# Optimization experiments

Measured on AMD Instinct MI355X. Metric: run time of the kernel, lower is better.

The kernel has to match this reference:

```python
import jax, jax.numpy as jnp
import numpy as np

I = 128  # input_size
B, T = 64, 512
SIZES = [(I, 2*I), (2*I, 4*I), (4*I, 8*I), (8*I, 4*I), (4*I, 2*I), (2*I, I)]


def gru_layer(x, Wih, Whh):
    # x: [B,T,Din], Wih: [3H,Din], Whh: [3H,H]. PyTorch GRU, bias=False, h0=0.
    Bb, Tt, _ = x.shape
    H = Whh.shape[1]
    xg = jnp.einsum('bti,gi->btg', x, Wih)  # precompute input projections [B,T,3H]

    def step(h, xt):
        hg = h @ Whh.T                      # [B,3H]
        xr, xz, xn = jnp.split(xt, 3, axis=-1)
        hr, hz, hn = jnp.split(hg, 3, axis=-1)
        r = jax.nn.sigmoid(xr + hr)
        z = jax.nn.sigmoid(xz + hz)
        n = jnp.tanh(xn + r * hn)
        h_new = (1.0 - z) * n + z * h
        return h_new, h_new

    h0 = jnp.zeros((Bb, H), x.dtype)
    _, ys = jax.lax.scan(step, h0, jnp.swapaxes(xg, 0, 1))  # [T,B,H]
    return jnp.swapaxes(ys, 0, 1)


def layer_norm(x, g, b):
    # eps=0 as in the original module
    m = jnp.mean(x, axis=-1, keepdims=True)
    v = jnp.mean(jnp.square(x - m), axis=-1, keepdims=True)
    return (x - m) * jax.lax.rsqrt(v) * g + b


def setup_inputs() -> dict:
    key = jax.random.key(0)
    keys = jax.random.split(key, 1 + 2 * len(SIZES))
    inp = {'x': jax.random.normal(keys[0], (B, T, I), dtype=jnp.float32)}
    for l, (din, h) in enumerate(SIZES):
        s_ih = 1.0 / np.sqrt(h)
        inp[f'Wih{l}'] = jax.random.uniform(keys[1 + 2 * l], (3 * h, din), jnp.float32, -s_ih, s_ih)
        inp[f'Whh{l}'] = jax.random.uniform(keys[2 + 2 * l], (3 * h, h), jnp.float32, -s_ih, s_ih)
        inp[f'g{l}'] = jnp.ones((h,), jnp.float32)
        inp[f'b{l}'] = jnp.zeros((h,), jnp.float32)
    return inp


def reference(x,
              Wih0, Whh0, g0, b0,
              Wih1, Whh1, g1, b1,
              Wih2, Whh2, g2, b2,
              Wih3, Whh3, g3, b3,
              Wih4, Whh4, g4, b4,
              Wih5, Whh5, g5, b5):
    h = x
    params = [(Wih0, Whh0, g0, b0), (Wih1, Whh1, g1, b1), (Wih2, Whh2, g2, b2),
              (Wih3, Whh3, g3, b3), (Wih4, Whh4, g4, b4), (Wih5, Whh5, g5, b5)]
    for Wih, Whh, g, b in params:
        h = layer_norm(gru_layer(h, Wih, Whh), g, b)
    return h
```

## Files before the change

### kernel.cpp

```cpp
#include <hip/hip_runtime.h>
#include <stdint.h>

#define TT 512
#define BB 64
#define MM (BB * TT)

typedef short bf16x8 __attribute__((ext_vector_type(8)));
typedef float f32x4  __attribute__((ext_vector_type(4)));

#define LNP ((size_t)MM * 1024)

__device__ __align__(256) float g_xg[(size_t)MM * 3072];
__device__ __align__(256) unsigned short g_hex[176160768];
__device__ __align__(256) unsigned short g_ln[2 * LNP];
__device__ __align__(256) unsigned short g_w[18579456];
__device__ unsigned g_cnt[6 * TT * 8 * 16];

__device__ __forceinline__ float bf2f(unsigned short u) {
  union { unsigned int i; float f; } c; c.i = ((unsigned int)u) << 16; return c.f;
}
__device__ __forceinline__ unsigned short f2bf(float f) {
  union { float f; unsigned int i; } c; c.f = f;
  unsigned int u = c.i;
  return (unsigned short)((u + 0x7FFFu + ((u >> 16) & 1u)) >> 16);
}

__device__ __forceinline__ void gload16(const void* g, void* l) {
  __builtin_amdgcn_global_load_lds(
      (const __attribute__((address_space(1))) unsigned int*)g,
      (__attribute__((address_space(3))) unsigned int*)l, 16, 0, 0);
}

__global__ void __launch_bounds__(256) k_zero() {
  int i = blockIdx.x * 256 + threadIdx.x;
  int st = gridDim.x * 256;
  for (; i < 6 * TT * 8 * 16; i += st) g_cnt[i] = 0;
}

__global__ void __launch_bounds__(256) k_cvt_split(const float* __restrict__ s, int n,
                                                   int offh, int offl) {
  int i = blockIdx.x * 256 + threadIdx.x;
  int st = gridDim.x * 256;
  for (; i < n; i += st) {
    float v = s[i];
    unsigned short hi = f2bf(v);
    g_w[offh + i] = hi;
    g_w[offl + i] = f2bf(v - bf2f(hi));
  }
}
__global__ void __launch_bounds__(256) k_cvt_x(const float* __restrict__ s, int n) {
  int i = blockIdx.x * 256 + threadIdx.x;
  int st = gridDim.x * 256;
  for (; i < n; i += st) {
    float v = s[i];
    unsigned short hi = f2bf(v);
    g_ln[i] = hi;
    g_ln[LNP + i] = f2bf(v - bf2f(hi));
  }
}

__global__ void __launch_bounds__(256) k_gemm(int N, int K, int bhoff, int bloff) {
  __shared__ char sm[65536];
  char* Ah = sm;
  char* Al = sm + 16384;
  char* Bh = sm + 32768;
  char* Bl = sm + 49152;
  const unsigned short* A0 = g_ln;
  const unsigned short* A1 = g_ln + LNP;
  const unsigned short* B0 = g_w + bhoff;
  const unsigned short* B1 = g_w + bloff;
  const int tid = threadIdx.x;
  const int lane = tid & 63;
  const int w = tid >> 6;
  const int wm = w >> 1, wn = w & 1;
  const int m0 = blockIdx.x * 128, n0 = blockIdx.y * 128;
  const int c16 = lane & 15, r4 = lane >> 4;

  f32x4 acc[4][4];
#pragma unroll
  for (int i = 0; i < 4; ++i)
#pragma unroll
    for (int j = 0; j < 4; ++j) acc[i][j] = {0.f, 0.f, 0.f, 0.f};

  for (int k0 = 0; k0 < K; k0 += 64) {
    __syncthreads();
#pragma unroll
    for (int i = 0; i < 4; ++i) {
      int c = i * 256 + tid;
      int row = c >> 3, ch = c & 7;
      size_t ao = (size_t)(m0 + row) * K + k0 + ch * 8;
      size_t bo = (size_t)(n0 + row) * K + k0 + ch * 8;
      gload16(A0 + ao, Ah + c * 16);
      gload16(A1 + ao, Al + c * 16);
      gload16(B0 + bo, Bh + c * 16);
      gload16(B1 + bo, Bl + c * 16);
    }
    __syncthreads();
#pragma unroll
    for (int ks = 0; ks < 2; ++ks) {
      bf16x8 avh[4], avl[4], bvh[4], bvl[4];
#pragma unroll
      for (int mt = 0; mt < 4; ++mt) {
        int o = (wm * 64 + mt * 16 + c16) * 128 + ks * 64 + r4 * 16;
        avh[mt] = *(const bf16x8*)(Ah + o);
        avl[mt] = *(const bf16x8*)(Al + o);
      }
#pragma unroll
      for (int nt = 0; nt < 4; ++nt) {
        int o = (wn * 64 + nt * 16 + c16) * 128 + ks * 64 + r4 * 16;
        bvh[nt] = *(const bf16x8*)(Bh + o);
        bvl[nt] = *(const bf16x8*)(Bl + o);
      }
#pragma unroll
      for (int mt = 0; mt < 4; ++mt)
#pragma unroll
        for (int nt = 0; nt < 4; ++nt) {
          acc[mt][nt] = __builtin_amdgcn_mfma_f32_16x16x32_bf16(avh[mt], bvh[nt], acc[mt][nt], 0, 0, 0);
          acc[mt][nt] = __builtin_amdgcn_mfma_f32_16x16x32_bf16(avl[mt], bvh[nt], acc[mt][nt], 0, 0, 0);
          acc[mt][nt] = __builtin_amdgcn_mfma_f32_16x16x32_bf16(avh[mt], bvl[nt], acc[mt][nt], 0, 0, 0);
        }
    }
  }
#pragma unroll
  for (int mt = 0; mt < 4; ++mt)
#pragma unroll
    for (int nt = 0; nt < 4; ++nt) {
      int col = n0 + wn * 64 + nt * 16 + c16;
#pragma unroll
      for (int q = 0; q < 4; ++q) {
        int row = m0 + wm * 64 + mt * 16 + r4 * 4 + q;
        g_xg[(size_t)row * N + col] = acc[mt][nt][q];
      }
    }
}

template <int H, int NCOL, int NBLK, int NG>
__global__ void __launch_bounds__(256) k_scan(int whoff, int wloff,
                                              unsigned long long hoff, int coff) {
  constexpr int RB = 2 * H;
  constexpr int KI = H / 32;
  constexpr int ROWS = 3 * NCOL;
  constexpr int PL = ROWS * RB;
  constexpr unsigned TGT = NBLK / NG;
  __shared__ char lds[2 * PL];
  unsigned short* hexh = g_hex + hoff;
  unsigned short* hexl = hexh + (size_t)TT * BB * H;
  const int tid = threadIdx.x;
  const int lane = tid & 63;
  const int w = tid >> 6;
  const int bid = blockIdx.x;
  const int jb = bid * NCOL;
  const int c16 = lane & 15, r4 = lane >> 4;

  {
    constexpr int CPR = RB / 16;
    const unsigned short* wh = g_w + whoff;
    const unsigned short* wl = g_w + wloff;
    for (int c = tid; c < ROWS * CPR; c += 256) {
      int r = c / CPR, ch = c % CPR;
      int p = r / NCOL, j = r % NCOL;
      size_t so = (size_t)(p * H + jb + j) * H + ch * 8;
      int byte = (ch * 16) ^ ((r & 7) << 4);
      *(float4*)(lds + r * RB + byte) = *(const float4*)(wh + so);
      *(float4*)(lds + PL + r * RB + byte) = *(const float4*)(wl + so);
    }
  }
  __syncthreads();

  float hprev[4] = {0.f, 0.f, 0.f, 0.f};
  const int rA = c16 & (NCOL - 1);
  const int grp = bid & (NG - 1);

  for (int t = 0; t < TT; ++t) {
    float xr[4], xz[4], xn[4];
    if (NCOL == 16 || c16 < NCOL) {
#pragma unroll
      for (int q = 0; q < 4; ++q) {
        int b = w * 16 + r4 * 4 + q;
        size_t xo = ((size_t)b * TT + t) * (3 * H) + jb + c16;
        xr[q] = g_xg[xo];
        xz[q] = g_xg[xo + H];
        xn[q] = g_xg[xo + 2 * H];
      }
    } else {
#pragma unroll
      for (int q = 0; q < 4; ++q) { xr[q] = 0.f; xz[q] = 0.f; xn[q] = 0.f; }
    }

    f32x4 acc[3];
#pragma unroll
    for (int g = 0; g < 3; ++g) acc[g] = {0.f, 0.f, 0.f, 0.f};

    if (t > 0) {
      if (tid < 64) {
        const unsigned* cp = g_cnt + ((size_t)(coff + t - 1) * 8) * 16;
        for (;;) {
          unsigned v = (lane < NG)
              ? __hip_atomic_load(cp + lane * 16, __ATOMIC_RELAXED, __HIP_MEMORY_SCOPE_AGENT)
              : TGT;
          if (__all(v >= TGT)) break;
        }
      }
      __builtin_amdgcn_fence(__ATOMIC_ACQUIRE, "agent");
      __syncthreads();

      const unsigned short* hrh = hexh + ((size_t)(t - 1) * BB + (w * 16 + c16)) * H + r4 * 8;
      const unsigned short* hrl = hexl + ((size_t)(t - 1) * BB + (w * 16 + c16)) * H + r4 * 8;
#pragma unroll 4
      for (int ki = 0; ki < KI; ++ki) {
        bf16x8 ah = *(const bf16x8*)(hrh + ki * 32);
        bf16x8 al = *(const bf16x8*)(hrl + ki * 32);
#pragma unroll
        for (int g = 0; g < 3; ++g) {
          const int row = g * NCOL + rA;
          const int ko = (ki * 64 + r4 * 16) ^ ((row & 7) << 4);
          const char* bp = lds + row * RB + ko;
          bf16x8 bh = *(const bf16x8*)bp;
          bf16x8 bl = *(const bf16x8*)(bp + PL);
          acc[g] = __builtin_amdgcn_mfma_f32_16x16x32_bf16(ah, bh, acc[g], 0, 0, 0);
          acc[g] = __builtin_amdgcn_mfma_f32_16x16x32_bf16(al, bh, acc[g], 0, 0, 0);
          acc[g] = __builtin_amdgcn_mfma_f32_16x16x32_bf16(ah, bl, acc[g], 0, 0, 0);
        }
      }
    }

    if (NCOL == 16 || c16 < NCOL) {
#pragma unroll
      for (int q = 0; q < 4; ++q) {
        int b = w * 16 + r4 * 4 + q;
        float rg = 1.f / (1.f + __expf(-(xr[q] + acc[0][q])));
        float zg = 1.f / (1.f + __expf(-(xz[q] + acc[1][q])));
        float ng = tanhf(xn[q] + rg * acc[2][q]);
        float h = (1.f - zg) * ng + zg * hprev[q];
        hprev[q] = h;
        size_t ho = ((size_t)t * BB + b) * H + jb + c16;
        unsigned short hi = f2bf(h);
        __builtin_nontemporal_store(hi, &hexh[ho]);
        __builtin_nontemporal_store(f2bf(h - bf2f(hi)), &hexl[ho]);
      }
    }
    __syncthreads();
    if (tid == 0)
      (void)__hip_atomic_fetch_add(g_cnt + ((size_t)(coff + t) * 8 + grp) * 16, 1u,
                                   __ATOMIC_RELEASE, __HIP_MEMORY_SCOPE_AGENT);
  }
}

template <int H, bool LAST>
__global__ void __launch_bounds__(256) k_ln(const float* __restrict__ gw,
                                            const float* __restrict__ bw,
                                            float* __restrict__ of32,
                                            unsigned long long hoff) {
  const int r = blockIdx.x * 4 + (threadIdx.x >> 6);
  const int lane = threadIdx.x & 63;
  const int b = r >> 9;
  const int t = r & 511;
  const unsigned short* row = g_hex + hoff + ((size_t)t * BB + b) * H;
  const unsigned short* rowl = row + (size_t)TT * BB * H;
  constexpr int E = H / 64;
  float x[E];
  if constexpr (E == 16) {
#pragma unroll
    for (int jj = 0; jj < 2; ++jj) {
      bf16x8 v = *(const bf16x8*)(row + (lane + jj * 64) * 8);
      bf16x8 u = *(const bf16x8*)(rowl + (lane + jj * 64) * 8);
#pragma unroll
      for (int e = 0; e < 8; ++e) x[jj * 8 + e] = bf2f((unsigned short)v[e]) + bf2f((unsigned short)u[e]);
    }
  } else if constexpr (E == 8) {
    bf16x8 v = *(const bf16x8*)(row + lane * 8);
    bf16x8 u = *(const bf16x8*)(rowl + lane * 8);
#pragma unroll
    for (int e = 0; e < 8; ++e) x[e] = bf2f((unsigned short)v[e]) + bf2f((unsigned short)u[e]);
  } else if constexpr (E == 4) {
    typedef short bf16x4 __attribute__((ext_vector_type(4)));
    bf16x4 v = *(const bf16x4*)(row + lane * 4);
    bf16x4 u = *(const bf16x4*)(rowl + lane * 4);
#pragma unroll
    for (int e = 0; e < 4; ++e) x[e] = bf2f((unsigned short)v[e]) + bf2f((unsigned short)u[e]);
  } else {
    typedef short bf16x2 __attribute__((ext_vector_type(2)));
    bf16x2 v = *(const bf16x2*)(row + lane * 2);
    bf16x2 u = *(const bf16x2*)(rowl + lane * 2);
#pragma unroll
    for (int e = 0; e < 2; ++e) x[e] = bf2f((unsigned short)v[e]) + bf2f((unsigned short)u[e]);
  }
  float s = 0.f;
#pragma unroll
  for (int e = 0; e < E; ++e) s += x[e];
#pragma unroll
  for (int m = 1; m < 64; m <<= 1) s += __shfl_xor(s, m);
  const float mean = s * (1.f / H);
  float vs = 0.f;
#pragma unroll
  for (int e = 0; e < E; ++e) { float d = x[e] - mean; vs += d * d; }
#pragma unroll
  for (int m = 1; m < 64; m <<= 1) vs += __shfl_xor(vs, m);
  const float rstd = rsqrtf(vs * (1.f / H));
#pragma unroll
  for (int e = 0; e < E; ++e) {
    int col;
    if constexpr (E == 16) col = (lane + (e >> 3) * 64) * 8 + (e & 7);
    else col = lane * E + e;
    float y = (x[e] - mean) * rstd * gw[col] + bw[col];
    if constexpr (LAST) {
      of32[(size_t)r * H + col] = y;
    } else {
      unsigned short hi = f2bf(y);
      g_ln[(size_t)r * H + col] = hi;
      g_ln[LNP + (size_t)r * H + col] = f2bf(y - bf2f(hi));
    }
  }
}

extern "C" void kernel_launch(void* const* d_in, const int* in_sizes, int n_in,
                              void* d_out, int out_size, void* d_ws, size_t ws_size,
                              hipStream_t stream) {
  (void)in_sizes; (void)n_in; (void)out_size; (void)d_ws; (void)ws_size;
  static const int DIN[6] = {128, 256, 512, 1024, 512, 256};
  static const int HS[6]  = {256, 512, 1024, 512, 256, 128};
  const int M = MM;

  int wihh_off[6], wihl_off[6], whhh_off[6], whhl_off[6];
  unsigned long long hex_off[6];
  {
    int off = 0;
    unsigned long long hoff = 0;
    for (int l = 0; l < 6; ++l) {
      int sih = 3 * HS[l] * DIN[l], shh = 3 * HS[l] * HS[l];
      wihh_off[l] = off; off += sih;
      wihl_off[l] = off; off += sih;
      whhh_off[l] = off; off += shh;
      whhl_off[l] = off; off += shh;
      hex_off[l] = hoff; hoff += 2ull * TT * BB * HS[l];
    }
  }

  k_zero<<<384, 256, 0, stream>>>();
  k_cvt_x<<<1024, 256, 0, stream>>>((const float*)d_in[0], M * 128);
  for (int l = 0; l < 6; ++l) {
    k_cvt_split<<<512, 256, 0, stream>>>((const float*)d_in[1 + 4 * l], 3 * HS[l] * DIN[l],
                                         wihh_off[l], wihl_off[l]);
    k_cvt_split<<<512, 256, 0, stream>>>((const float*)d_in[2 + 4 * l], 3 * HS[l] * HS[l],
                                         whhh_off[l], whhl_off[l]);
  }

  for (int l = 0; l < 6; ++l) {
    const int H = HS[l], K = DIN[l], N = 3 * H;
    dim3 gg(M / 128, N / 128);
    k_gemm<<<gg, 256, 0, stream>>>(N, K, wihh_off[l], wihl_off[l]);

    const int coff = l * TT;
    switch (H) {
      case 1024: k_scan<1024, 4, 256, 8><<<256, 256, 0, stream>>>(whhh_off[l], whhl_off[l], hex_off[l], coff); break;
      case 512:  k_scan<512, 8, 64, 4><<<64, 256, 0, stream>>>(whhh_off[l], whhl_off[l], hex_off[l], coff); break;
      case 256:  k_scan<256, 16, 16, 2><<<16, 256, 0, stream>>>(whhh_off[l], whhl_off[l], hex_off[l], coff); break;
      case 128:  k_scan<128, 16, 8, 2><<<8, 256, 0, stream>>>(whhh_off[l], whhl_off[l], hex_off[l], coff); break;
    }

    const float* gp = (const float*)d_in[3 + 4 * l];
    const float* bp = (const float*)d_in[4 + 4 * l];
    if (l == 5) {
      k_ln<128, true><<<M / 4, 256, 0, stream>>>(gp, bp, (float*)d_out, hex_off[l]);
    } else {
      switch (H) {
        case 1024: k_ln<1024, false><<<M / 4, 256, 0, stream>>>(gp, bp, nullptr, hex_off[l]); break;
        case 512:  k_ln<512, false><<<M / 4, 256, 0, stream>>>(gp, bp, nullptr, hex_off[l]); break;
        case 256:  k_ln<256, false><<<M / 4, 256, 0, stream>>>(gp, bp, nullptr, hex_off[l]); break;
      }
    }
  }
}
```

Measured before the change: 34.37 ms.

## Pack hidden hi/lo into one word, use per-block flags, stream weights from global

The recurrent scan now packs the bf16 hi and lo halves of each hidden value into one 32-bit word, written and read with relaxed agent-scope atomics. The grouped counter barrier is replaced by per-block flags that a single wave polls. Each block always handles 16 columns, so fewer blocks run for H=1024 and H=512. Recurrent weights are read straight from global memory instead of being staged in LDS. The aim is to cut per-step synchronisation and hidden-state traffic, at the risk of more global weight loads per step and weaker memory ordering since the acquire/release fences are gone.

```diff
diff --git a/kernel.cpp b/kernel.cpp
--- a/kernel.cpp
+++ b/kernel.cpp
@@ -7,14 +7,16 @@
 
 typedef short bf16x8 __attribute__((ext_vector_type(8)));
 typedef float f32x4  __attribute__((ext_vector_type(4)));
+typedef unsigned uint32x4 __attribute__((ext_vector_type(4)));
+typedef unsigned uint32x2 __attribute__((ext_vector_type(2)));
 
 #define LNP ((size_t)MM * 1024)
 
 __device__ __align__(256) float g_xg[(size_t)MM * 3072];
-__device__ __align__(256) unsigned short g_hex[176160768];
+__device__ __align__(256) unsigned g_hex[88080384];
 __device__ __align__(256) unsigned short g_ln[2 * LNP];
 __device__ __align__(256) unsigned short g_w[18579456];
-__device__ unsigned g_cnt[6 * TT * 8 * 16];
+__device__ unsigned g_flags[6 * TT * 64];
 
 __device__ __forceinline__ float bf2f(unsigned short u) {
   union { unsigned int i; float f; } c; c.i = ((unsigned int)u) << 16; return c.f;
@@ -34,7 +36,7 @@
 __global__ void __launch_bounds__(256) k_zero() {
   int i = blockIdx.x * 256 + threadIdx.x;
   int st = gridDim.x * 256;
-  for (; i < 6 * TT * 8 * 16; i += st) g_cnt[i] = 0;
+  for (; i < 6 * TT * 64; i += st) g_flags[i] = 0;
 }
 
 __global__ void __launch_bounds__(256) k_cvt_split(const float* __restrict__ s, int n,
@@ -134,57 +136,35 @@
     }
 }
 
-template <int H, int NCOL, int NBLK, int NG>
-__global__ void __launch_bounds__(256) k_scan(int whoff, int wloff,
-                                              unsigned long long hoff, int coff) {
-  constexpr int RB = 2 * H;
+template <int H, int NBLK>
+__global__ void __launch_bounds__(256) k_scan(int whoff, int wloff, size_t hoff, int coff) {
   constexpr int KI = H / 32;
-  constexpr int ROWS = 3 * NCOL;
-  constexpr int PL = ROWS * RB;
-  constexpr unsigned TGT = NBLK / NG;
-  __shared__ char lds[2 * PL];
-  unsigned short* hexh = g_hex + hoff;
-  unsigned short* hexl = hexh + (size_t)TT * BB * H;
+  unsigned* hexc = g_hex + hoff;
   const int tid = threadIdx.x;
   const int lane = tid & 63;
   const int w = tid >> 6;
   const int bid = blockIdx.x;
-  const int jb = bid * NCOL;
+  const int jb = bid * 16;
   const int c16 = lane & 15, r4 = lane >> 4;
 
-  {
-    constexpr int CPR = RB / 16;
-    const unsigned short* wh = g_w + whoff;
-    const unsigned short* wl = g_w + wloff;
-    for (int c = tid; c < ROWS * CPR; c += 256) {
-      int r = c / CPR, ch = c % CPR;
-      int p = r / NCOL, j = r % NCOL;
-      size_t so = (size_t)(p * H + jb + j) * H + ch * 8;
-      int byte = (ch * 16) ^ ((r & 7) << 4);
-      *(float4*)(lds + r * RB + byte) = *(const float4*)(wh + so);
-      *(float4*)(lds + PL + r * RB + byte) = *(const float4*)(wl + so);
-    }
-  }
-  __syncthreads();
+  const unsigned short* bh0 = g_w + whoff + ((size_t)(0 * H + jb + c16)) * H + r4 * 8;
+  const unsigned short* bh1 = g_w + whoff + ((size_t)(1 * H + jb + c16)) * H + r4 * 8;
+  const unsigned short* bh2 = g_w + whoff + ((size_t)(2 * H + jb + c16)) * H + r4 * 8;
+  const long wld = (long)wloff - (long)whoff;
+
+  const int arow = w * 16 + c16;
 
   float hprev[4] = {0.f, 0.f, 0.f, 0.f};
-  const int rA = c16 & (NCOL - 1);
-  const int grp = bid & (NG - 1);
 
   for (int t = 0; t < TT; ++t) {
     float xr[4], xz[4], xn[4];
-    if (NCOL == 16 || c16 < NCOL) {
-#pragma unroll
-      for (int q = 0; q < 4; ++q) {
-        int b = w * 16 + r4 * 4 + q;
-        size_t xo = ((size_t)b * TT + t) * (3 * H) + jb + c16;
-        xr[q] = g_xg[xo];
-        xz[q] = g_xg[xo + H];
-        xn[q] = g_xg[xo + 2 * H];
-      }
-    } else {
-#pragma unroll
-      for (int q = 0; q < 4; ++q) { xr[q] = 0.f; xz[q] = 0.f; xn[q] = 0.f; }
+#pragma unroll
+    for (int q = 0; q < 4; ++q) {
+      int b = w * 16 + r4 * 4 + q;
+      size_t xo = ((size_t)b * TT + t) * (3 * H) + jb + c16;
+      xr[q] = g_xg[xo];
+      xz[q] = g_xg[xo + H];
+      xn[q] = g_xg[xo + 2 * H];
     }
 
     f32x4 acc[3];
@@ -193,56 +173,76 @@
 
     if (t > 0) {
       if (tid < 64) {
-        const unsigned* cp = g_cnt + ((size_t)(coff + t - 1) * 8) * 16;
-        for (;;) {
-          unsigned v = (lane < NG)
-              ? __hip_atomic_load(cp + lane * 16, __ATOMIC_RELAXED, __HIP_MEMORY_SCOPE_AGENT)
-              : TGT;
-          if (__all(v >= TGT)) break;
-        }
-      }
-      __builtin_amdgcn_fence(__ATOMIC_ACQUIRE, "agent");
+        const unsigned* fl = g_flags + (size_t)(coff + t - 1) * 64;
+        unsigned v;
+        do {
+          v = (lane < NBLK)
+              ? __hip_atomic_load(fl + lane, __ATOMIC_RELAXED, __HIP_MEMORY_SCOPE_AGENT)
+              : 1u;
+        } while (__any(v == 0));
+      }
       __syncthreads();
 
-      const unsigned short* hrh = hexh + ((size_t)(t - 1) * BB + (w * 16 + c16)) * H + r4 * 8;
-      const unsigned short* hrl = hexl + ((size_t)(t - 1) * BB + (w * 16 + c16)) * H + r4 * 8;
+      const unsigned long long* ap = reinterpret_cast<const unsigned long long*>(
+          hexc + ((size_t)(t - 1) * BB + arow) * H + r4 * 8);
 #pragma unroll 4
       for (int ki = 0; ki < KI; ++ki) {
-        bf16x8 ah = *(const bf16x8*)(hrh + ki * 32);
-        bf16x8 al = *(const bf16x8*)(hrl + ki * 32);
-#pragma unroll
-        for (int g = 0; g < 3; ++g) {
-          const int row = g * NCOL + rA;
-          const int ko = (ki * 64 + r4 * 16) ^ ((row & 7) << 4);
-          const char* bp = lds + row * RB + ko;
-          bf16x8 bh = *(const bf16x8*)bp;
-          bf16x8 bl = *(const bf16x8*)(bp + PL);
-          acc[g] = __builtin_amdgcn_mfma_f32_16x16x32_bf16(ah, bh, acc[g], 0, 0, 0);
-          acc[g] = __builtin_amdgcn_mfma_f32_16x16x32_bf16(al, bh, acc[g], 0, 0, 0);
-          acc[g] = __builtin_amdgcn_mfma_f32_16x16x32_bf16(ah, bl, acc[g], 0, 0, 0);
-        }
-      }
-    }
-
-    if (NCOL == 16 || c16 < NCOL) {
-#pragma unroll
-      for (int q = 0; q < 4; ++q) {
-        int b = w * 16 + r4 * 4 + q;
-        float rg = 1.f / (1.f + __expf(-(xr[q] + acc[0][q])));
-        float zg = 1.f / (1.f + __expf(-(xz[q] + acc[1][q])));
-        float ng = tanhf(xn[q] + rg * acc[2][q]);
-        float h = (1.f - zg) * ng + zg * hprev[q];
-        hprev[q] = h;
-        size_t ho = ((size_t)t * BB + b) * H + jb + c16;
-        unsigned short hi = f2bf(h);
-        __builtin_nontemporal_store(hi, &hexh[ho]);
-        __builtin_nontemporal_store(f2bf(h - bf2f(hi)), &hexl[ho]);
-      }
-    }
+        unsigned long long d0 = __hip_atomic_load(ap + ki * 16 + 0, __ATOMIC_RELAXED, __HIP_MEMORY_SCOPE_AGENT);
+        unsigned long long d1 = __hip_atomic_load(ap + ki * 16 + 1, __ATOMIC_RELAXED, __HIP_MEMORY_SCOPE_AGENT);
+        unsigned long long d2 = __hip_atomic_load(ap + ki * 16 + 2, __ATOMIC_RELAXED, __HIP_MEMORY_SCOPE_AGENT);
+        unsigned long long d3 = __hip_atomic_load(ap + ki * 16 + 3, __ATOMIC_RELAXED, __HIP_MEMORY_SCOPE_AGENT);
+        unsigned u0 = (unsigned)d0, u1 = (unsigned)(d0 >> 32);
+        unsigned u2 = (unsigned)d1, u3 = (unsigned)(d1 >> 32);
+        unsigned u4 = (unsigned)d2, u5 = (unsigned)(d2 >> 32);
+        unsigned u6 = (unsigned)d3, u7 = (unsigned)(d3 >> 32);
+        union { uint32x4 u; bf16x8 v; } ch, cl;
+        ch.u[0] = (u1 & 0xffff0000u) | (u0 >> 16);
+        ch.u[1] = (u3 & 0xffff0000u) | (u2 >> 16);
+        ch.u[2] = (u5 & 0xffff0000u) | (u4 >> 16);
+        ch.u[3] = (u7 & 0xffff0000u) | (u6 >> 16);
+        cl.u[0] = (u1 << 16) | (u0 & 0xffffu);
+        cl.u[1] = (u3 << 16) | (u2 & 0xffffu);
+        cl.u[2] = (u5 << 16) | (u4 & 0xffffu);
+        cl.u[3] = (u7 << 16) | (u6 & 0xffffu);
+        bf16x8 ah = ch.v, al = cl.v;
+
+        bf16x8 b0h = *(const bf16x8*)(bh0 + ki * 32);
+        bf16x8 b0l = *(const bf16x8*)(bh0 + wld + ki * 32);
+        acc[0] = __builtin_amdgcn_mfma_f32_16x16x32_bf16(ah, b0h, acc[0], 0, 0, 0);
+        acc[0] = __builtin_amdgcn_mfma_f32_16x16x32_bf16(al, b0h, acc[0], 0, 0, 0);
+        acc[0] = __builtin_amdgcn_mfma_f32_16x16x32_bf16(ah, b0l, acc[0], 0, 0, 0);
+        bf16x8 b1h = *(const bf16x8*)(bh1 + ki * 32);
+        bf16x8 b1l = *(const bf16x8*)(bh1 + wld + ki * 32);
+        acc[1] = __builtin_amdgcn_mfma_f32_16x16x32_bf16(ah, b1h, acc[1], 0, 0, 0);
+        acc[1] = __builtin_amdgcn_mfma_f32_16x16x32_bf16(al, b1h, acc[1], 0, 0, 0);
+        acc[1] = __builtin_amdgcn_mfma_f32_16x16x32_bf16(ah, b1l, acc[1], 0, 0, 0);
+        bf16x8 b2h = *(const bf16x8*)(bh2 + ki * 32);
+        bf16x8 b2l = *(const bf16x8*)(bh2 + wld + ki * 32);
+        acc[2] = __builtin_amdgcn_mfma_f32_16x16x32_bf16(ah, b2h, acc[2], 0, 0, 0);
+        acc[2] = __builtin_amdgcn_mfma_f32_16x16x32_bf16(al, b2h, acc[2], 0, 0, 0);
+        acc[2] = __builtin_amdgcn_mfma_f32_16x16x32_bf16(ah, b2l, acc[2], 0, 0, 0);
+      }
+    }
+
+#pragma unroll
+    for (int q = 0; q < 4; ++q) {
+      int b = w * 16 + r4 * 4 + q;
+      float rg = 1.f / (1.f + __expf(-(xr[q] + acc[0][q])));
+      float zg = 1.f / (1.f + __expf(-(xz[q] + acc[1][q])));
+      float ng = tanhf(xn[q] + rg * acc[2][q]);
+      float h = (1.f - zg) * ng + zg * hprev[q];
+      hprev[q] = h;
+      unsigned short hi = f2bf(h);
+      unsigned short lo = f2bf(h - bf2f(hi));
+      unsigned pu = ((unsigned)hi << 16) | (unsigned)lo;
+      __hip_atomic_store(hexc + ((size_t)t * BB + b) * H + jb + c16, pu,
+                         __ATOMIC_RELAXED, __HIP_MEMORY_SCOPE_AGENT);
+    }
+    __builtin_amdgcn_s_waitcnt(0);
     __syncthreads();
     if (tid == 0)
-      (void)__hip_atomic_fetch_add(g_cnt + ((size_t)(coff + t) * 8 + grp) * 16, 1u,
-                                   __ATOMIC_RELEASE, __HIP_MEMORY_SCOPE_AGENT);
+      __hip_atomic_store(g_flags + (size_t)(coff + t) * 64 + bid, 1u,
+                         __ATOMIC_RELAXED, __HIP_MEMORY_SCOPE_AGENT);
   }
 }
 
@@ -250,40 +250,26 @@
 __global__ void __launch_bounds__(256) k_ln(const float* __restrict__ gw,
                                             const float* __restrict__ bw,
                                             float* __restrict__ of32,
-                                            unsigned long long hoff) {
+                                            size_t hoff) {
   const int r = blockIdx.x * 4 + (threadIdx.x >> 6);
   const int lane = threadIdx.x & 63;
   const int b = r >> 9;
   const int t = r & 511;
-  const unsigned short* row = g_hex + hoff + ((size_t)t * BB + b) * H;
-  const unsigned short* rowl = row + (size_t)TT * BB * H;
+  const unsigned* row = g_hex + hoff + ((size_t)t * BB + b) * H;
   constexpr int E = H / 64;
   float x[E];
-  if constexpr (E == 16) {
-#pragma unroll
-    for (int jj = 0; jj < 2; ++jj) {
-      bf16x8 v = *(const bf16x8*)(row + (lane + jj * 64) * 8);
-      bf16x8 u = *(const bf16x8*)(rowl + (lane + jj * 64) * 8);
-#pragma unroll
-      for (int e = 0; e < 8; ++e) x[jj * 8 + e] = bf2f((unsigned short)v[e]) + bf2f((unsigned short)u[e]);
-    }
-  } else if constexpr (E == 8) {
-    bf16x8 v = *(const bf16x8*)(row + lane * 8);
-    bf16x8 u = *(const bf16x8*)(rowl + lane * 8);
-#pragma unroll
-    for (int e = 0; e < 8; ++e) x[e] = bf2f((unsigned short)v[e]) + bf2f((unsigned short)u[e]);
-  } else if constexpr (E == 4) {
-    typedef short bf16x4 __attribute__((ext_vector_type(4)));
-    bf16x4 v = *(const bf16x4*)(row + lane * 4);
-    bf16x4 u = *(const bf16x4*)(rowl + lane * 4);
-#pragma unroll
-    for (int e = 0; e < 4; ++e) x[e] = bf2f((unsigned short)v[e]) + bf2f((unsigned short)u[e]);
+  if constexpr (E >= 4) {
+#pragma unroll
+    for (int j = 0; j < E / 4; ++j) {
+      uint32x4 v = *(const uint32x4*)(row + lane * E + 4 * j);
+#pragma unroll
+      for (int e = 0; e < 4; ++e)
+        x[4 * j + e] = bf2f((unsigned short)(v[e] >> 16)) + bf2f((unsigned short)(v[e] & 0xffffu));
+    }
   } else {
-    typedef short bf16x2 __attribute__((ext_vector_type(2)));
-    bf16x2 v = *(const bf16x2*)(row + lane * 2);
-    bf16x2 u = *(const bf16x2*)(rowl + lane * 2);
-#pragma unroll
-    for (int e = 0; e < 2; ++e) x[e] = bf2f((unsigned short)v[e]) + bf2f((unsigned short)u[e]);
+    uint32x2 v = *(const uint32x2*)(row + lane * 2);
+    x[0] = bf2f((unsigned short)(v[0] >> 16)) + bf2f((unsigned short)(v[0] & 0xffffu));
+    x[1] = bf2f((unsigned short)(v[1] >> 16)) + bf2f((unsigned short)(v[1] & 0xffffu));
   }
   float s = 0.f;
 #pragma unroll
@@ -299,9 +285,7 @@
   const float rstd = rsqrtf(vs * (1.f / H));
 #pragma unroll
   for (int e = 0; e < E; ++e) {
-    int col;
-    if constexpr (E == 16) col = (lane + (e >> 3) * 64) * 8 + (e & 7);
-    else col = lane * E + e;
+    int col = lane * E + e;
     float y = (x[e] - mean) * rstd * gw[col] + bw[col];
     if constexpr (LAST) {
       of32[(size_t)r * H + col] = y;
@@ -322,17 +306,17 @@
   const int M = MM;
 
   int wihh_off[6], wihl_off[6], whhh_off[6], whhl_off[6];
-  unsigned long long hex_off[6];
+  size_t hex_off[6];
   {
     int off = 0;
-    unsigned long long hoff = 0;
+    size_t hoff = 0;
     for (int l = 0; l < 6; ++l) {
       int sih = 3 * HS[l] * DIN[l], shh = 3 * HS[l] * HS[l];
       wihh_off[l] = off; off += sih;
       wihl_off[l] = off; off += sih;
       whhh_off[l] = off; off += shh;
       whhl_off[l] = off; off += shh;
-      hex_off[l] = hoff; hoff += 2ull * TT * BB * HS[l];
+      hex_off[l] = hoff; hoff += (size_t)TT * BB * HS[l];
     }
   }
 
@@ -352,10 +336,10 @@
 
     const int coff = l * TT;
     switch (H) {
-      case 1024: k_scan<1024, 4, 256, 8><<<256, 256, 0, stream>>>(whhh_off[l], whhl_off[l], hex_off[l], coff); break;
-      case 512:  k_scan<512, 8, 64, 4><<<64, 256, 0, stream>>>(whhh_off[l], whhl_off[l], hex_off[l], coff); break;
-      case 256:  k_scan<256, 16, 16, 2><<<16, 256, 0, stream>>>(whhh_off[l], whhl_off[l], hex_off[l], coff); break;
-      case 128:  k_scan<128, 16, 8, 2><<<8, 256, 0, stream>>>(whhh_off[l], whhl_off[l], hex_off[l], coff); break;
+      case 1024: k_scan<1024, 64><<<64, 256, 0, stream>>>(whhh_off[l], whhl_off[l], hex_off[l], coff); break;
+      case 512:  k_scan<512, 32><<<32, 256, 0, stream>>>(whhh_off[l], whhl_off[l], hex_off[l], coff); break;
+      case 256:  k_scan<256, 16><<<16, 256, 0, stream>>>(whhh_off[l], whhl_off[l], hex_off[l], coff); break;
+      case 128:  k_scan<128, 8><<<8, 256, 0, stream>>>(whhh_off[l], whhl_off[l], hex_off[l], coff); break;
     }
 
     const float* gp = (const float*)d_in[3 + 4 * l];
```

After: 59.77 ms. 1.74x slower.
